# Optimization experiments

Measured on AMD Instinct MI355X. Metric: run time of the kernel, lower is better.

## Reference

```python
import math
import jax, jax.numpy as jnp
import numpy as np

DIM = 256; DEPTH = 5; FANOUT = 10; VOCAB = 257
B = 16; T = 2048
NEXP = 8; HID = 512; TOPK = 2; TEMP = 1.0; HEADS = 2
CAPACITY = math.ceil(B * TOPK / NEXP * 1.1)  # capacity-based dispatch, =5
LAYER_SIZES = [FANOUT ** l for l in range(DEPTH)]  # [1,10,100,1000,10000]


def setup_inputs() -> dict:
    key = jax.random.key(0)
    ks = iter(jax.random.split(key, 64))
    def p(shape, scale=0.02):
        return jax.random.normal(next(ks), shape, jnp.float32) * scale
    inp = {
        'tokens': jax.random.randint(next(ks), (B, T), 0, VOCAB),
        'embed': p((VOCAB, DIM)),
        'pin_w': p((DIM, DIM)), 'pin_b': jnp.zeros(DIM, jnp.float32),
        'pch_w': p((DIM, DIM)), 'pch_b': jnp.zeros(DIM, jnp.float32),
        'depth_bias': p((DEPTH, DIM)),
        'q_w': p((DIM, DIM)), 'q_b': jnp.zeros(DIM, jnp.float32),
        'k_w': p((DIM, DIM)), 'k_b': jnp.zeros(DIM, jnp.float32),
        'v_w': p((DIM, DIM)), 'v_b': jnp.zeros(DIM, jnp.float32),
        'o_w': p((DIM, DIM)), 'o_b': jnp.zeros(DIM, jnp.float32),
        'level_gate': jnp.zeros(DEPTH, jnp.float32),
        'depth_gate': jnp.zeros((DEPTH, DIM), jnp.float32),
        'in_proj_w': p((DIM, 3 * DIM)), 'in_proj_b': jnp.zeros(3 * DIM, jnp.float32),
        'out_proj_w': p((DIM, DIM)), 'out_proj_b': jnp.zeros(DIM, jnp.float32),
        'ln_g': jnp.ones(DIM, jnp.float32), 'ln_b': jnp.zeros(DIM, jnp.float32),
        'ic_gate': jnp.zeros(1, jnp.float32),
        'gate_w': p((DIM, NEXP)), 'gate_b': jnp.zeros(NEXP, jnp.float32),
        'ew1': p((NEXP, DIM, HID)), 'eb1': jnp.zeros((NEXP, HID), jnp.float32),
        'ew2': p((NEXP, HID, DIM)), 'eb2': jnp.zeros((NEXP, DIM), jnp.float32),
        'hw1': p((DIM, DIM)), 'hb1': jnp.zeros(DIM, jnp.float32),
        'hw2': p((DIM, VOCAB)), 'hb2': jnp.zeros(VOCAB, jnp.float32),
    }
    return inp


def _fractal(context, pin_w, pin_b, pch_w, pch_b, depth_bias, q_w, q_b, k_w, k_b,
             v_w, v_b, o_w, o_b, level_gate, depth_gate,
             in_proj_w, in_proj_b, out_proj_w, out_proj_b, ln_g, ln_b, ic_gate):
    Bc = context.shape[0]
    base = context @ pin_w + pin_b                       # [B,D]
    y_next = None
    level_means = [None] * DEPTH
    inv_sqrt_d = 1.0 / math.sqrt(DIM)
    for l in reversed(range(DEPTH)):
        n = LAYER_SIZES[l]
        if l == DEPTH - 1:
            child_agg = jnp.zeros((Bc, n, DIM), context.dtype)
        else:
            yg = y_next.reshape(Bc, n, FANOUT, DIM)      # children grouped per parent
            q = (base + depth_bias[l]) @ q_w + q_b       # [B,D], shared across nodes
            k = yg @ k_w + k_b
            v = yg @ v_w + v_b
            att = jax.nn.softmax(jnp.einsum('bd,bnfd->bnf', q, k) * inv_sqrt_d, axis=-1)
            child_agg = jax.nn.sigmoid(depth_gate[l]) * jnp.einsum('bnf,bnfd->bnd', att, v)
        gate = jax.nn.sigmoid(level_gate[l])
        upd = (base[:, None, :] + depth_bias[l][None, None, :] + child_agg @ pch_w + pch_b) * gate
        y = jax.nn.relu(upd) @ o_w + o_b                 # [B,n,D]
        level_means[l] = y.mean(axis=1)
        y_next = y
    root = y_next[:, 0, :]                               # n==1 at level 0
    # interconnect: MHA over per-level means [B,DEPTH,D]
    z = jnp.stack(level_means, axis=1)
    qkv = z @ in_proj_w + in_proj_b
    qh, kh, vh = jnp.split(qkv, 3, axis=-1)
    hd = DIM // HEADS
    def to_heads(t):
        return t.reshape(Bc, DEPTH, HEADS, hd).transpose(0, 2, 1, 3)
    qh, kh, vh = to_heads(qh), to_heads(kh), to_heads(vh)
    aw = jax.nn.softmax(jnp.einsum('bhqd,bhkd->bhqk', qh, kh) / math.sqrt(hd), axis=-1)
    z2 = jnp.einsum('bhqk,bhkd->bhqd', aw, vh).transpose(0, 2, 1, 3).reshape(Bc, DEPTH, DIM)
    z2 = z2 @ out_proj_w + out_proj_b
    zs = z + z2
    mu = zs.mean(-1, keepdims=True)
    var = ((zs - mu) ** 2).mean(-1, keepdims=True)
    zn = (zs - mu) / jnp.sqrt(var + 1e-5) * ln_g + ln_b
    return root + jax.nn.sigmoid(ic_gate) * zn[:, 0, :]


def _moe(ctx, gate_w, gate_b, ew1, eb1, ew2, eb2):
    scaled = (ctx @ gate_w + gate_b) / TEMP
    top_vals, top_idx = jax.lax.top_k(scaled, TOPK)      # [B,K]
    gs = jax.nn.softmax(top_vals, axis=-1)               # [B,K], strictly > 0
    out = jnp.zeros_like(ctx)
    for e in range(NEXP):                                # fixed small expert loop
        sflat = jnp.where(top_idx == e, gs, -1.0).reshape(-1)   # [B*K]
        vals, pos = jax.lax.top_k(sflat, CAPACITY)       # capacity-limited dispatch
        w = jnp.where(vals > 0.0, vals, 0.0)             # drop unassigned/overflow
        tok = pos // TOPK
        xin = ctx[tok]                                   # [cap,D]
        eo = jax.nn.relu(xin @ ew1[e] + eb1[e]) @ ew2[e] + eb2[e]
        out = out.at[tok].add(eo * w[:, None])
    return out


def reference(tokens, embed, pin_w, pin_b, pch_w, pch_b, depth_bias,
              q_w, q_b, k_w, k_b, v_w, v_b, o_w, o_b, level_gate, depth_gate,
              in_proj_w, in_proj_b, out_proj_w, out_proj_b, ln_g, ln_b, ic_gate,
              gate_w, gate_b, ew1, eb1, ew2, eb2, hw1, hb1, hw2, hb2):
    x = embed[tokens]                                    # [B,T,D]
    context = x.mean(axis=1)                             # [B,D]
    root = _fractal(context, pin_w, pin_b, pch_w, pch_b, depth_bias, q_w, q_b,
                    k_w, k_b, v_w, v_b, o_w, o_b, level_gate, depth_gate,
                    in_proj_w, in_proj_b, out_proj_w, out_proj_b, ln_g, ln_b, ic_gate)
    root = root + _moe(root, gate_w, gate_b, ew1, eb1, ew2, eb2)
    h = x + root[:, None, :]                             # per-token logits from context + token emb
    logits = jax.nn.relu(h @ hw1 + hb1) @ hw2 + hb2      # [B,T,V]
    return logits
```

## Files before the change

### kernel.cpp

```cpp
#include <hip/hip_runtime.h>
#include <hip/hip_bf16.h>
#include <math.h>

#define DIM    256
#define DEPTH  5
#define FANOUT 10
#define VOCAB  257
#define BB     16
#define TT     2048
#define NEXP   8
#define HID    512
#define TOPK   2
#define CAP    5

__device__ __forceinline__ float sigm(float x) { return 1.f / (1.f + expf(-x)); }

__device__ __forceinline__ void mv8x2(const float* sv, const float* __restrict__ W,
                                      int kseg, int cq, float red[16][DIM]) {
  const float* Wp = W + (size_t)kseg * 16 * DIM + cq * 4;
  float4 acc = {0.f, 0.f, 0.f, 0.f};
#pragma unroll 1
  for (int h = 0; h < 2; ++h) {
    float4 wv[8];
#pragma unroll
    for (int i = 0; i < 8; ++i)
      wv[i] = *(const float4*)(Wp + (size_t)(h * 8 + i) * DIM);
#pragma unroll
    for (int i = 0; i < 8; ++i) {
      float s = sv[kseg * 16 + h * 8 + i];
      acc.x = fmaf(s, wv[i].x, acc.x);
      acc.y = fmaf(s, wv[i].y, acc.y);
      acc.z = fmaf(s, wv[i].z, acc.z);
      acc.w = fmaf(s, wv[i].w, acc.w);
    }
    __builtin_amdgcn_sched_barrier(0);
  }
  *(float4*)&red[kseg][cq * 4] = acc;
}

__device__ __forceinline__ float sum16(const float red[16][DIM], int d) {
  float s = 0.f;
#pragma unroll
  for (int g = 0; g < 16; ++g) s += red[g][d];
  return s;
}

__global__ void __launch_bounds__(1024) k_fractal(
    const int* __restrict__ tokens, const float* __restrict__ embed,
    const float* __restrict__ pin_w, const float* __restrict__ pin_b,
    const float* __restrict__ pch_w, const float* __restrict__ pch_b,
    const float* __restrict__ depth_bias,
    const float* __restrict__ v_w, const float* __restrict__ v_b,
    const float* __restrict__ o_w, const float* __restrict__ o_b,
    const float* __restrict__ level_gate, const float* __restrict__ depth_gate,
    const float* __restrict__ in_proj_w, const float* __restrict__ in_proj_b,
    const float* __restrict__ out_proj_w, const float* __restrict__ out_proj_b,
    const float* __restrict__ ln_g, const float* __restrict__ ln_b,
    const float* __restrict__ ic_gate,
    float* __restrict__ rootA, float* __restrict__ root2,
    int* __restrict__ bidx, int* __restrict__ boff) {
  int b = blockIdx.x;
  int tid = threadIdx.x;
  int d = tid & 255;
  int ks = tid >> 8;
  int k0 = ks * 64;
  int kseg = tid >> 6;
  int cq = tid & 63;
  __shared__ int cnt[VOCAB];
  __shared__ float sv[DIM];
  __shared__ float basev[DIM];
  __shared__ float ym[DEPTH][DIM];
  __shared__ float q0v[DIM], kh[DEPTH][DIM], vh[DEPTH][DIM];
  __shared__ float red11[4][11][DIM];
  __shared__ float zsv[DIM];
  __shared__ float aw[16];
  __shared__ float redl[8];
  __shared__ int offb[VOCAB + 1];
  __shared__ int woff[VOCAB];
  float (*red16)[DIM] = reinterpret_cast<float(*)[DIM]>(&red11[0][0][0]);

  for (int i = tid; i < VOCAB; i += 1024) cnt[i] = 0;
  __syncthreads();
  for (int t = tid; t < TT; t += 1024) atomicAdd(&cnt[tokens[b * TT + t]], 1);
  __syncthreads();
  {
    const float* Ep = embed + (size_t)kseg * 16 * DIM + cq * 4;
    float4 acc = {0.f, 0.f, 0.f, 0.f};
#pragma unroll 1
    for (int h = 0; h < 2; ++h) {
      float4 ev[8];
#pragma unroll
      for (int i = 0; i < 8; ++i)
        ev[i] = *(const float4*)(Ep + (size_t)(h * 8 + i) * DIM);
#pragma unroll
      for (int i = 0; i < 8; ++i) {
        float cv = (float)cnt[kseg * 16 + h * 8 + i];
        acc.x = fmaf(cv, ev[i].x, acc.x);
        acc.y = fmaf(cv, ev[i].y, acc.y);
        acc.z = fmaf(cv, ev[i].z, acc.z);
        acc.w = fmaf(cv, ev[i].w, acc.w);
      }
      __builtin_amdgcn_sched_barrier(0);
    }
    *(float4*)&red16[kseg][cq * 4] = acc;
  }
  __syncthreads();
  if (ks == 0) {
    float s = sum16(red16, d);
    s = fmaf((float)cnt[256], embed[(size_t)256 * DIM + d], s);
    sv[d] = s * (1.0f / (float)TT);
  }
  __syncthreads();

  mv8x2(sv, pin_w, kseg, cq, red16);
  __syncthreads();
  if (ks == 0) {
    float base = sum16(red16, d) + pin_b[d];
    basev[d] = base;
    float u = (base + depth_bias[4 * DIM + d] + pch_b[d]) * sigm(level_gate[4]);
    sv[d] = fmaxf(u, 0.f);
  }
  __syncthreads();
  mv8x2(sv, o_w, kseg, cq, red16);
  __syncthreads();
  if (ks == 0) {
    float y = sum16(red16, d) + o_b[d];
    ym[4][d] = y;
    sv[d] = y;
  }
  __syncthreads();
  for (int l = 3; l >= 0; --l) {
    mv8x2(sv, v_w, kseg, cq, red16);
    __syncthreads();
    if (ks == 0) {
      float vv = sum16(red16, d) + v_b[d];
      sv[d] = sigm(depth_gate[l * DIM + d]) * vv;
    }
    __syncthreads();
    mv8x2(sv, pch_w, kseg, cq, red16);
    __syncthreads();
    if (ks == 0) {
      float t = sum16(red16, d) + pch_b[d];
      float u = (basev[d] + depth_bias[l * DIM + d] + t) * sigm(level_gate[l]);
      sv[d] = fmaxf(u, 0.f);
    }
    __syncthreads();
    mv8x2(sv, o_w, kseg, cq, red16);
    __syncthreads();
    if (ks == 0) {
      float y = sum16(red16, d) + o_b[d];
      ym[l][d] = y;
      sv[d] = y;
    }
    __syncthreads();
  }
  {
    float aq = 0.f;
    float ak0 = 0.f, ak1 = 0.f, ak2 = 0.f, ak3 = 0.f, ak4 = 0.f;
    float av0 = 0.f, av1 = 0.f, av2 = 0.f, av3 = 0.f, av4 = 0.f;
#pragma unroll
    for (int h = 0; h < 8; ++h) {
      int kb = k0 + h * 8;
      float wq[8], wk[8], wv8[8];
#pragma unroll
      for (int i = 0; i < 8; ++i) {
        const float* wrow = in_proj_w + (size_t)(kb + i) * 768;
        wq[i] = wrow[d]; wk[i] = wrow[256 + d]; wv8[i] = wrow[512 + d];
      }
#pragma unroll
      for (int i = 0; i < 8; ++i) {
        float z0 = ym[0][kb + i];
        aq  = fmaf(z0, wq[i], aq);
        ak0 = fmaf(z0, wk[i], ak0);
        av0 = fmaf(z0, wv8[i], av0);
        float z1 = ym[1][kb + i];
        ak1 = fmaf(z1, wk[i], ak1);
        av1 = fmaf(z1, wv8[i], av1);
        float z2 = ym[2][kb + i];
        ak2 = fmaf(z2, wk[i], ak2);
        av2 = fmaf(z2, wv8[i], av2);
        float z3 = ym[3][kb + i];
        ak3 = fmaf(z3, wk[i], ak3);
        av3 = fmaf(z3, wv8[i], av3);
        float z4 = ym[4][kb + i];
        ak4 = fmaf(z4, wk[i], ak4);
        av4 = fmaf(z4, wv8[i], av4);
      }
    }
    red11[ks][0][d] = ak0; red11[ks][1][d] = ak1; red11[ks][2][d] = ak2;
    red11[ks][3][d] = ak3; red11[ks][4][d] = ak4;
    red11[ks][5][d] = av0; red11[ks][6][d] = av1; red11[ks][7][d] = av2;
    red11[ks][8][d] = av3; red11[ks][9][d] = av4;
    red11[ks][10][d] = aq;
  }
  __syncthreads();
  for (int idx = tid; idx < 11 * DIM; idx += 1024) {
    int c = idx >> 8, dd = idx & 255;
    float sum = red11[0][c][dd] + red11[1][c][dd] + red11[2][c][dd] + red11[3][c][dd];
    if (c < 5)       kh[c][dd]     = sum + in_proj_b[256 + dd];
    else if (c < 10) vh[c - 5][dd] = sum + in_proj_b[512 + dd];
    else             q0v[dd]       = sum + in_proj_b[dd];
  }
  __syncthreads();
  {
    int wid = tid >> 6;
    if (wid < 10) {
      int h = wid / 5, l = wid - h * 5;
      int lane = tid & 63;
      float s = q0v[h * 128 + lane] * kh[l][h * 128 + lane];
      s = fmaf(q0v[h * 128 + 64 + lane], kh[l][h * 128 + 64 + lane], s);
      for (int o = 32; o > 0; o >>= 1) s += __shfl_down(s, o, 64);
      if (lane == 0) aw[wid] = s * 0.08838834764831845f;
    }
  }
  __syncthreads();
  if (tid < 2) {
    float m = aw[tid * 5];
    for (int l = 1; l < 5; ++l) m = fmaxf(m, aw[tid * 5 + l]);
    float e[5], ssum = 0.f;
    for (int l = 0; l < 5; ++l) { e[l] = expf(aw[tid * 5 + l] - m); ssum += e[l]; }
    for (int l = 0; l < 5; ++l) aw[tid * 5 + l] = e[l] / ssum;
  }
  __syncthreads();
  if (ks == 0) {
    int h = d >> 7;
    float z2 = 0.f;
    for (int l = 0; l < 5; ++l) z2 = fmaf(aw[h * 5 + l], vh[l][d], z2);
    sv[d] = z2;
  }
  __syncthreads();
  mv8x2(sv, out_proj_w, kseg, cq, red16);
  __syncthreads();
  if (ks == 0) {
    float z2p = sum16(red16, d) + out_proj_b[d];
    zsv[d] = ym[0][d] + z2p;
  }
  __syncthreads();
  float zs = 0.f, df = 0.f, mu = 0.f;
  if (tid < 256) {
    zs = zsv[tid];
    float v = zs;
    for (int o = 32; o > 0; o >>= 1) v += __shfl_down(v, o, 64);
    if ((tid & 63) == 0) redl[tid >> 6] = v;
  }
  __syncthreads();
  if (tid < 256) {
    mu = (redl[0] + redl[1] + redl[2] + redl[3]) * (1.f / 256.f);
    df = zs - mu;
  }
  __syncthreads();
  if (tid < 256) {
    float v = df * df;
    for (int o = 32; o > 0; o >>= 1) v += __shfl_down(v, o, 64);
    if ((tid & 63) == 0) redl[tid >> 6] = v;
  }
  __syncthreads();
  if (tid < 256) {
    float var = (redl[0] + redl[1] + redl[2] + redl[3]) * (1.f / 256.f);
    float zn = df / sqrtf(var + 1e-5f) * ln_g[tid] + ln_b[tid];
    float r = ym[0][tid] + sigm(ic_gate[0]) * zn;
    rootA[b * DIM + tid] = r;
    root2[b * DIM + tid] = r;
  }
  __syncthreads();
  if (tid == 0) {
    int a = 0;
    for (int v = 0; v < VOCAB; ++v) { offb[v] = a; a += cnt[v]; }
    offb[VOCAB] = a;
  }
  __syncthreads();
  if (tid <= VOCAB) boff[b * (VOCAB + 1) + tid] = offb[tid];
  if (tid < VOCAB) woff[tid] = offb[tid];
  __syncthreads();
  for (int t = tid; t < TT; t += 1024) {
    int tok = tokens[b * TT + t];
    int p = atomicAdd(&woff[tok], 1);
    bidx[b * TT + p] = t;
  }
}

__global__ void __launch_bounds__(256) k_moe(
    const float* __restrict__ rootA,
    const float* __restrict__ gate_w, const float* __restrict__ gate_b,
    const float* __restrict__ ew1, const float* __restrict__ eb1,
    const float* __restrict__ ew2, const float* __restrict__ eb2,
    float* __restrict__ root2) {
  int bx = blockIdx.x;
  int e = bx >> 3, jt = bx & 7, j0 = jt * 64;
  int tid = threadIdx.x, w = tid >> 6, lane = tid & 63;
  __shared__ float rlds[BB * DIM];
  __shared__ float gwlds[DIM * NEXP];
  __shared__ float xin[CAP][DIM];
  __shared__ float red[CAP][4][64];
  __shared__ float hloc[CAP][64];
  __shared__ float sc[BB * NEXP];
  __shared__ float gs[BB * TOPK];
  __shared__ int gidx[BB * TOPK];
  __shared__ int stok[CAP];
  __shared__ float swt[CAP];
  for (int idx = tid; idx < BB * DIM / 4; idx += 256)
    *(float4*)&rlds[idx * 4] = *(const float4*)&rootA[idx * 4];
  for (int idx = tid; idx < DIM * NEXP / 4; idx += 256)
    *(float4*)&gwlds[idx * 4] = *(const float4*)&gate_w[idx * 4];
  __syncthreads();
  if (tid < BB * NEXP) {
    int b = tid >> 3, ep = tid & 7;
    float chunk[8];
#pragma unroll
    for (int g = 0; g < 8; ++g) {
      float acc = 0.f;
#pragma unroll 8
      for (int i = 0; i < 32; ++i) {
        int k = g * 32 + i;
        acc = fmaf(rlds[b * DIM + k], gwlds[k * NEXP + ep], acc);
      }
      chunk[g] = acc;
    }
    float s = gate_b[ep];
#pragma unroll
    for (int g = 0; g < 8; ++g) s += chunk[g];
    sc[tid] = s;
  }
  __syncthreads();
  if (tid < BB) {
    int bb = tid;
    int i0 = 0; float v0 = sc[bb * 8 + 0];
    for (int ee = 1; ee < 8; ++ee) { float v = sc[bb * 8 + ee]; if (v > v0) { v0 = v; i0 = ee; } }
    int i1 = -1; float v1 = -1e30f;
    for (int ee = 0; ee < 8; ++ee) {
      if (ee == i0) continue;
      float v = sc[bb * 8 + ee];
      if (v > v1) { v1 = v; i1 = ee; }
    }
    float e1v = expf(v1 - v0);
    float s = 1.f + e1v;
    gs[bb * 2 + 0] = 1.f / s;  gidx[bb * 2 + 0] = i0;
    gs[bb * 2 + 1] = e1v / s;  gidx[bb * 2 + 1] = i1;
  }
  __syncthreads();
  if (tid == 0) {
    unsigned used = 0u;
    for (int s = 0; s < CAP; ++s) {
      int bi = 0; float bv = -1e30f;
      for (int i = 0; i < 32; ++i) {
        if (used & (1u << i)) continue;
        float v = (gidx[i] == e) ? gs[i] : -1.0f;
        if (v > bv) { bv = v; bi = i; }
      }
      used |= (1u << bi);
      stok[s] = bi >> 1;
      swt[s] = bv > 0.f ? bv : 0.f;
    }
  }
  __syncthreads();
  for (int idx = tid; idx < CAP * DIM; idx += 256) {
    int s = idx >> 8, k = idx & 255;
    xin[s][k] = rlds[stok[s] * DIM + k];
  }
  __syncthreads();
  {
    float a0 = 0.f, a1 = 0.f, a2 = 0.f, a3 = 0.f, a4 = 0.f;
    const float* W = ew1 + (size_t)e * DIM * HID + j0 + lane;
    int kbase = w * 64;
#pragma unroll
    for (int h = 0; h < 8; ++h) {
      float wv[8];
#pragma unroll
      for (int i = 0; i < 8; ++i) wv[i] = W[(size_t)(kbase + h * 8 + i) * HID];
#pragma unroll
      for (int i = 0; i < 8; ++i) {
        int k = kbase + h * 8 + i;
        a0 = fmaf(xin[0][k], wv[i], a0);
        a1 = fmaf(xin[1][k], wv[i], a1);
        a2 = fmaf(xin[2][k], wv[i], a2);
        a3 = fmaf(xin[3][k], wv[i], a3);
        a4 = fmaf(xin[4][k], wv[i], a4);
      }
    }
    red[0][w][lane] = a0; red[1][w][lane] = a1; red[2][w][lane] = a2;
    red[3][w][lane] = a3; red[4][w][lane] = a4;
  }
  __syncthreads();
  for (int idx = tid; idx < CAP * 64; idx += 256) {
    int s = idx >> 6, j = idx & 63;
    float sum = red[s][0][j] + red[s][1][j] + red[s][2][j] + red[s][3][j]
              + eb1[e * HID + j0 + j];
    hloc[s][j] = fmaxf(sum, 0.f);
  }
  __syncthreads();
  {
    int d = tid;
    float a0 = 0.f, a1 = 0.f, a2 = 0.f, a3 = 0.f, a4 = 0.f;
    const float* W2 = ew2 + (size_t)e * HID * DIM + (size_t)j0 * DIM + d;
#pragma unroll
    for (int h = 0; h < 8; ++h) {
      float wv[8];
#pragma unroll
      for (int i = 0; i < 8; ++i) wv[i] = W2[(size_t)(h * 8 + i) * DIM];
#pragma unroll
      for (int i = 0; i < 8; ++i) {
        int j = h * 8 + i;
        a0 = fmaf(hloc[0][j], wv[i], a0);
        a1 = fmaf(hloc[1][j], wv[i], a1);
        a2 = fmaf(hloc[2][j], wv[i], a2);
        a3 = fmaf(hloc[3][j], wv[i], a3);
        a4 = fmaf(hloc[4][j], wv[i], a4);
      }
    }
    float bias = (jt == 0) ? eb2[e * DIM + d] : 0.f;
    float pa[1];
    (void)pa;
#pragma unroll
    for (int s = 0; s < CAP; ++s) {
      float as = (s == 0) ? a0 : (s == 1) ? a1 : (s == 2) ? a2 : (s == 3) ? a3 : a4;
      float wgt = swt[s];
      if (wgt > 0.f)
        atomicAdd(&root2[stok[s] * DIM + d], (as + bias) * wgt);
    }
  }
}

__global__ void __launch_bounds__(256) k_logits(
    const float* __restrict__ embed, const float* __restrict__ root2,
    const float* __restrict__ hw1, const float* __restrict__ hb1,
    const float* __restrict__ hw2, const float* __restrict__ hb2,
    const int* __restrict__ bidx, const int* __restrict__ boff,
    float* __restrict__ out) {
  int tok = blockIdx.x, r0 = blockIdx.y * 4;
  int c = threadIdx.x;
  __shared__ float hrow[4][DIM];
  __shared__ float hid[4][DIM];
  __shared__ float tailred[4][17];
  __shared__ float tailv[4];
  {
    float ev = embed[(size_t)tok * DIM + c];
#pragma unroll
    for (int j = 0; j < 4; ++j) hrow[j][c] = ev + root2[(size_t)(r0 + j) * DIM + c];
  }
  __syncthreads();
  {
    float a0 = hb1[c], a1 = a0, a2 = a0, a3 = a0;
    for (int kb = 0; kb < DIM; kb += 8) {
      float wv[8];
#pragma unroll
      for (int i = 0; i < 8; ++i) wv[i] = hw1[(size_t)(kb + i) * DIM + c];
#pragma unroll
      for (int i = 0; i < 8; ++i) {
        int k = kb + i;
        a0 = fmaf(hrow[0][k], wv[i], a0);
        a1 = fmaf(hrow[1][k], wv[i], a1);
        a2 = fmaf(hrow[2][k], wv[i], a2);
        a3 = fmaf(hrow[3][k], wv[i], a3);
      }
    }
    hid[0][c] = fmaxf(a0, 0.f); hid[1][c] = fmaxf(a1, 0.f);
    hid[2][c] = fmaxf(a2, 0.f); hid[3][c] = fmaxf(a3, 0.f);
  }
  __syncthreads();
  float a0, a1, a2, a3;
  {
    a0 = hb2[c]; a1 = a0; a2 = a0; a3 = a0;
    for (int kb = 0; kb < DIM; kb += 8) {
      float wv[8];
#pragma unroll
      for (int i = 0; i < 8; ++i) wv[i] = hw2[(size_t)(kb + i) * VOCAB + c];
#pragma unroll
      for (int i = 0; i < 8; ++i) {
        int k = kb + i;
        a0 = fmaf(hid[0][k], wv[i], a0);
        a1 = fmaf(hid[1][k], wv[i], a1);
        a2 = fmaf(hid[2][k], wv[i], a2);
        a3 = fmaf(hid[3][k], wv[i], a3);
      }
    }
  }
  if (c < 64) {
    int r = c >> 4, seg = c & 15;
    float sum = 0.f;
#pragma unroll 4
    for (int i = 0; i < 16; ++i) {
      int k = seg * 16 + i;
      sum = fmaf(hid[r][k], hw2[(size_t)k * VOCAB + 256], sum);
    }
    tailred[r][seg] = sum;
  }
  __syncthreads();
  if (c < 4) {
    float a = hb2[256];
#pragma unroll
    for (int s = 0; s < 16; ++s) a += tailred[c][s];
    tailv[c] = a;
  }
  __syncthreads();
#pragma unroll
  for (int j = 0; j < 4; ++j) {
    int b = r0 + j;
    int s = boff[b * (VOCAB + 1) + tok];
    int e = boff[b * (VOCAB + 1) + tok + 1];
    float aj = (j == 0) ? a0 : (j == 1) ? a1 : (j == 2) ? a2 : a3;
    float tl = tailv[j];
    for (int m = s; m < e; ++m) {
      int t = bidx[b * TT + m];
      size_t base = (size_t)(b * TT + t) * VOCAB;
      out[base + c] = aj;
      if (c == 0) out[base + 256] = tl;
    }
  }
}

extern "C" void kernel_launch(void* const* d_in, const int* in_sizes, int n_in,
                              void* d_out, int out_size, void* d_ws, size_t ws_size,
                              hipStream_t stream) {
  (void)in_sizes; (void)n_in; (void)out_size; (void)ws_size;
  const int*   tokens     = (const int*)d_in[0];
  const float* embed      = (const float*)d_in[1];
  const float* pin_w      = (const float*)d_in[2];
  const float* pin_b      = (const float*)d_in[3];
  const float* pch_w      = (const float*)d_in[4];
  const float* pch_b      = (const float*)d_in[5];
  const float* depth_bias = (const float*)d_in[6];
  const float* v_w        = (const float*)d_in[11];
  const float* v_b        = (const float*)d_in[12];
  const float* o_w        = (const float*)d_in[13];
  const float* o_b        = (const float*)d_in[14];
  const float* level_gate = (const float*)d_in[15];
  const float* depth_gate = (const float*)d_in[16];
  const float* in_proj_w  = (const float*)d_in[17];
  const float* in_proj_b  = (const float*)d_in[18];
  const float* out_proj_w = (const float*)d_in[19];
  const float* out_proj_b = (const float*)d_in[20];
  const float* ln_g       = (const float*)d_in[21];
  const float* ln_b       = (const float*)d_in[22];
  const float* ic_gate    = (const float*)d_in[23];
  const float* gate_w     = (const float*)d_in[24];
  const float* gate_b     = (const float*)d_in[25];
  const float* ew1        = (const float*)d_in[26];
  const float* eb1        = (const float*)d_in[27];
  const float* ew2        = (const float*)d_in[28];
  const float* eb2        = (const float*)d_in[29];
  const float* hw1        = (const float*)d_in[30];
  const float* hb1        = (const float*)d_in[31];
  const float* hw2        = (const float*)d_in[32];
  const float* hb2        = (const float*)d_in[33];
  float* out = (float*)d_out;

  float* ws      = (float*)d_ws;
  float* rootA   = ws + 4096;
  float* root2   = ws + 8192;
  int*   bidx    = (int*)(ws + 43136);
  int*   boff    = (int*)(ws + 75904);

  k_fractal<<<BB, 1024, 0, stream>>>(tokens, embed, pin_w, pin_b, pch_w, pch_b,
                                     depth_bias, v_w, v_b, o_w, o_b, level_gate,
                                     depth_gate, in_proj_w, in_proj_b, out_proj_w,
                                     out_proj_b, ln_g, ln_b, ic_gate, rootA, root2,
                                     bidx, boff);
  k_moe<<<NEXP * 8, 256, 0, stream>>>(rootA, gate_w, gate_b, ew1, eb1,
                                      ew2, eb2, root2);
  k_logits<<<dim3(VOCAB, 4), 256, 0, stream>>>(embed, root2, hw1, hb1, hw2, hb2,
                                               bidx, boff, out);
}
```

Baseline: 244.3 us.

## Add L2 prefetch blocks for weights and split token bucketing into separate blocks

Extra blocks are launched in the fractal kernel to read every weight matrix it uses into the L2 cache, and in the MoE kernel to read the expert weights, with the loaded values discarded. Token counting and bucket construction move out of the per-batch fractal blocks into their own 16 blocks, so that work runs in parallel with the serial fractal chain. The aim is to hide the latency of the serial matvec chain behind warm caches and added parallelism. The cost is redundant memory traffic and extra blocks competing for CUs, and the bucketing still recounts tokens.

```diff
diff --git a/kernel.cpp b/kernel.cpp
--- a/kernel.cpp
+++ b/kernel.cpp
@@ -59,13 +59,8 @@
     const float* __restrict__ ic_gate,
     float* __restrict__ rootA, float* __restrict__ root2,
     int* __restrict__ bidx, int* __restrict__ boff) {
-  int b = blockIdx.x;
+  int bx = blockIdx.x;
   int tid = threadIdx.x;
-  int d = tid & 255;
-  int ks = tid >> 8;
-  int k0 = ks * 64;
-  int kseg = tid >> 6;
-  int cq = tid & 63;
   __shared__ int cnt[VOCAB];
   __shared__ float sv[DIM];
   __shared__ float basev[DIM];
@@ -78,6 +73,56 @@
   __shared__ int offb[VOCAB + 1];
   __shared__ int woff[VOCAB];
   float (*red16)[DIM] = reinterpret_cast<float(*)[DIM]>(&red11[0][0][0]);
+
+  if (bx >= 2 * BB) {
+    int p = bx - 2 * BB;
+    int r = ((p >> 3) + (bx & 7)) % 36;
+    const float* W; size_t off;
+    if (r < 4)       { W = pin_w;      off = (size_t)r * 16384; }
+    else if (r < 8)  { W = pch_w;      off = (size_t)(r - 4) * 16384; }
+    else if (r < 12) { W = v_w;        off = (size_t)(r - 8) * 16384; }
+    else if (r < 16) { W = o_w;        off = (size_t)(r - 12) * 16384; }
+    else if (r < 20) { W = out_proj_w; off = (size_t)(r - 16) * 16384; }
+    else if (r < 32) { W = in_proj_w;  off = (size_t)(r - 20) * 16384; }
+    else             { W = embed;      off = (size_t)(r - 32) * 16384; }
+    const float4* src = (const float4*)(W + off) + tid;
+    float4 a = src[0], b4 = src[1024], c4 = src[2048], d4 = src[3072];
+    float sx = a.x + b4.x + c4.x + d4.x;
+    float sy = a.y + b4.y + c4.y + d4.y;
+    float sz = a.z + b4.z + c4.z + d4.z;
+    float sw = a.w + b4.w + c4.w + d4.w;
+    asm volatile("" :: "v"(sx), "v"(sy), "v"(sz), "v"(sw));
+    return;
+  }
+  if (bx >= BB) {
+    int b = bx - BB;
+    for (int i = tid; i < VOCAB; i += 1024) cnt[i] = 0;
+    __syncthreads();
+    for (int t = tid; t < TT; t += 1024) atomicAdd(&cnt[tokens[b * TT + t]], 1);
+    __syncthreads();
+    if (tid == 0) {
+      int a = 0;
+      for (int v = 0; v < VOCAB; ++v) { offb[v] = a; a += cnt[v]; }
+      offb[VOCAB] = a;
+    }
+    __syncthreads();
+    if (tid <= VOCAB) boff[b * (VOCAB + 1) + tid] = offb[tid];
+    if (tid < VOCAB) woff[tid] = offb[tid];
+    __syncthreads();
+    for (int t = tid; t < TT; t += 1024) {
+      int tok = tokens[b * TT + t];
+      int p = atomicAdd(&woff[tok], 1);
+      bidx[b * TT + p] = t;
+    }
+    return;
+  }
+
+  int b = bx;
+  int d = tid & 255;
+  int ks = tid >> 8;
+  int k0 = ks * 64;
+  int kseg = tid >> 6;
+  int cq = tid & 63;
 
   for (int i = tid; i < VOCAB; i += 1024) cnt[i] = 0;
   __syncthreads();
@@ -262,21 +307,6 @@
     rootA[b * DIM + tid] = r;
     root2[b * DIM + tid] = r;
   }
-  __syncthreads();
-  if (tid == 0) {
-    int a = 0;
-    for (int v = 0; v < VOCAB; ++v) { offb[v] = a; a += cnt[v]; }
-    offb[VOCAB] = a;
-  }
-  __syncthreads();
-  if (tid <= VOCAB) boff[b * (VOCAB + 1) + tid] = offb[tid];
-  if (tid < VOCAB) woff[tid] = offb[tid];
-  __syncthreads();
-  for (int t = tid; t < TT; t += 1024) {
-    int tok = tokens[b * TT + t];
-    int p = atomicAdd(&woff[tok], 1);
-    bidx[b * TT + p] = t;
-  }
 }
 
 __global__ void __launch_bounds__(256) k_moe(
@@ -286,8 +316,23 @@
     const float* __restrict__ ew2, const float* __restrict__ eb2,
     float* __restrict__ root2) {
   int bx = blockIdx.x;
+  int tid = threadIdx.x;
+  if (bx >= 64) {
+    int r = (bx - 64) % 128;
+    const float* W = (r < 64) ? ew1 + (size_t)r * 16384
+                              : ew2 + (size_t)(r - 64) * 16384;
+    const float4* src = (const float4*)W + tid;
+    float sx = 0.f, sy = 0.f, sz = 0.f, sw = 0.f;
+#pragma unroll 4
+    for (int i = 0; i < 16; ++i) {
+      float4 v = src[i * 256];
+      sx += v.x; sy += v.y; sz += v.z; sw += v.w;
+    }
+    asm volatile("" :: "v"(sx), "v"(sy), "v"(sz), "v"(sw));
+    return;
+  }
   int e = bx >> 3, jt = bx & 7, j0 = jt * 64;
-  int tid = threadIdx.x, w = tid >> 6, lane = tid & 63;
+  int w = tid >> 6, lane = tid & 63;
   __shared__ float rlds[BB * DIM];
   __shared__ float gwlds[DIM * NEXP];
   __shared__ float xin[CAP][DIM];
@@ -408,8 +453,6 @@
       }
     }
     float bias = (jt == 0) ? eb2[e * DIM + d] : 0.f;
-    float pa[1];
-    (void)pa;
 #pragma unroll
     for (int s = 0; s < CAP; ++s) {
       float as = (s == 0) ? a0 : (s == 1) ? a1 : (s == 2) ? a2 : (s == 3) ? a3 : a4;
@@ -550,13 +593,13 @@
   int*   bidx    = (int*)(ws + 43136);
   int*   boff    = (int*)(ws + 75904);
 
-  k_fractal<<<BB, 1024, 0, stream>>>(tokens, embed, pin_w, pin_b, pch_w, pch_b,
-                                     depth_bias, v_w, v_b, o_w, o_b, level_gate,
-                                     depth_gate, in_proj_w, in_proj_b, out_proj_w,
-                                     out_proj_b, ln_g, ln_b, ic_gate, rootA, root2,
-                                     bidx, boff);
-  k_moe<<<NEXP * 8, 256, 0, stream>>>(rootA, gate_w, gate_b, ew1, eb1,
-                                      ew2, eb2, root2);
+  k_fractal<<<256, 1024, 0, stream>>>(tokens, embed, pin_w, pin_b, pch_w, pch_b,
+                                      depth_bias, v_w, v_b, o_w, o_b, level_gate,
+                                      depth_gate, in_proj_w, in_proj_b, out_proj_w,
+                                      out_proj_b, ln_g, ln_b, ic_gate, rootA, root2,
+                                      bidx, boff);
+  k_moe<<<256, 256, 0, stream>>>(rootA, gate_w, gate_b, ew1, eb1,
+                                 ew2, eb2, root2);
   k_logits<<<dim3(VOCAB, 4), 256, 0, stream>>>(embed, root2, hw1, hb1, hw2, hb2,
                                                bidx, boff, out);
 }
```

New measurement: 234.3 us. 4.1% less time.
